# Kernel tuning notes

Measured on AMD Instinct MI355X. Metric: run time of the kernel, lower is better.

The kernel has to match this reference:

```python
import jax, jax.numpy as jnp
import numpy as np

B, N, D_IN, D_HID, D_OUT = 64, 512, 512, 512, 512


def setup_inputs() -> dict:
    key = jax.random.key(0)
    ks = jax.random.split(key, 8)
    gain = 0.02  # xavier_normal_ gain used in reset_parameters_xavier

    def xavier(k, fan_in, fan_out):
        std = gain * np.sqrt(2.0 / (fan_in + fan_out))
        return jax.random.normal(k, (fan_in, fan_out), dtype=jnp.float32) * std

    return {
        "batch_graph": jax.random.normal(ks[0], (B, N, D_IN), dtype=jnp.float32),
        "adj": jax.random.uniform(ks[1], (B, N, N), dtype=jnp.float32),
        "W1": xavier(ks[2], D_IN, D_HID),
        "b1": jnp.zeros((D_HID,), dtype=jnp.float32),
        "W2": xavier(ks[3], D_HID, D_HID),
        "b2": jnp.zeros((D_HID,), dtype=jnp.float32),
        "W3": xavier(ks[4], D_HID, D_OUT),
        "b3": jnp.zeros((D_OUT,), dtype=jnp.float32),
    }


def _normalize_adj(adj):
    # rowsum^-0.5 with inf -> 0 (original: torch.pow then isinf mask)
    rowsum = adj.sum(axis=1)                       # [B, N] (sum over dim 1, as in torch)
    safe = jnp.where(rowsum == 0, 1.0, rowsum)
    r = jnp.where(rowsum == 0, 0.0, safe ** -0.5)  # [B, N]
    # (adj @ D)^T @ D = D @ adj^T @ D with D = diag(r)
    return r[:, :, None] * jnp.swapaxes(adj, 1, 2) * r[:, None, :]


def reference(batch_graph, adj, W1, b1, W2, b2, W3, b3):
    # Block-diagonal big_adj @ big_graph == per-graph batched matmul.
    A = _normalize_adj(adj)  # [B, N, N]

    def gc(x, W, b):
        # support = x @ W ; output = A @ support + b
        return jnp.einsum('bij,bjd->bid', A, x @ W) + b

    # dropout is identity in eval mode (deterministic reference)
    x = jax.nn.relu(gc(batch_graph, W1, b1))
    x = jax.nn.relu(gc(x, W2, b2))
    return gc(x, W3, b3)  # [B, N, D_OUT]
```

## Files before the change

### kernel.cpp

```cpp
#include <hip/hip_runtime.h>
#include <cstdint>
#include <cstddef>

typedef _Float16 f16;
typedef _Float16 f16x4 __attribute__((ext_vector_type(4)));
typedef _Float16 f16x8 __attribute__((ext_vector_type(8)));
typedef float    f32x4 __attribute__((ext_vector_type(4)));

#define NB 64
#define NN 262144

__device__ __forceinline__ void gload_lds16(const void* g, void* l) {
    __builtin_amdgcn_global_load_lds(
        (const __attribute__((address_space(1))) void*)g,
        (__attribute__((address_space(3))) void*)l, 16, 0, 0);
}

__device__ __forceinline__ int SWC(int row, int col) {
    return ((((col >> 2) ^ (row >> 2)) & 15) << 2) | (col & 3);
}

__global__ __launch_bounds__(256)
void k_prep(const float* __restrict__ adj, f16* __restrict__ A_raw,
            float* __restrict__ part,
            const float* __restrict__ W1, const float* __restrict__ W2,
            const float* __restrict__ W3, f16* __restrict__ Wt,
            const float* __restrict__ X0, f16* __restrict__ Xa) {
    __shared__ __align__(16) float t[4096];
    __shared__ float red[4][64];
    const int tid = threadIdx.x;

    for (int u = blockIdx.x; u < 12480; u += 2048) {
        if (u >= 4288) {
            size_t i = ((size_t)(u - 4288) * 256 + tid) * 8;
            float4 v0 = *(const float4*)(X0 + i);
            float4 v1 = *(const float4*)(X0 + i + 4);
            f16x8 o;
            o[0] = (f16)v0.x; o[1] = (f16)v0.y; o[2] = (f16)v0.z; o[3] = (f16)v0.w;
            o[4] = (f16)v1.x; o[5] = (f16)v1.y; o[6] = (f16)v1.z; o[7] = (f16)v1.w;
            *(f16x8*)(Xa + i) = o;
        } else if (u < 4096) {
            const int xcd = u & 7, loc = u >> 3;
            const int b = xcd * 8 + (loc >> 6);
            const int tile = loc & 63;
            const int i0 = (tile >> 3) * 64, j0 = (tile & 7) * 64;
            const int jt = tile & 7;
            const float* ab = adj + (size_t)b * NN;
            #pragma unroll
            for (int s = 0; s < 4; ++s) {
                int rr = s * 16 + (tid >> 4);
                int creal = SWC(rr, (tid & 15) * 4);
                gload_lds16(&ab[(size_t)(j0 + rr) * 512 + i0 + creal],
                            &t[s * 1024 + tid * 4]);
            }
            asm volatile("s_waitcnt vmcnt(0)" ::: "memory");
            __syncthreads();
            {
                int c = tid & 63, g = tid >> 6;
                float sg = 0.f;
                #pragma unroll
                for (int s = 0; s < 16; ++s) {
                    int row = g * 16 + s;
                    sg += t[row * 64 + SWC(row, c)];
                }
                red[g][c] = sg;
            }
            f16* Ab = A_raw + (size_t)b * NN;
            int jq = (tid & 15) * 4;
            int ib = tid >> 4;
            #pragma unroll
            for (int s = 0; s < 4; ++s) {
                int ii = ib + s * 16;
                f16x4 o;
                #pragma unroll
                for (int q = 0; q < 4; ++q)
                    o[q] = (f16)t[(jq + q) * 64 + SWC(jq + q, ii)];
                *(f16x4*)&Ab[(size_t)(i0 + ii) * 512 + j0 + jq] = o;
            }
            __syncthreads();
            if (tid < 64)
                part[((size_t)b * 8 + jt) * 512 + i0 + tid] =
                    red[0][tid] + red[1][tid] + red[2][tid] + red[3][tid];
            __syncthreads();
        } else {
            int cb = u - 4096;
            int z = cb >> 6, rem = cb & 63;
            const float* W = z == 0 ? W1 : (z == 1 ? W2 : W3);
            f16* out = Wt + (size_t)z * NN;
            int k0 = (rem >> 3) * 64, d0 = (rem & 7) * 64;
            int c = tid & 63, r4 = tid >> 6;
            #pragma unroll
            for (int s = 0; s < 16; ++s) {
                int rr = r4 + s * 4;
                t[rr * 64 + SWC(rr, c)] = W[(size_t)(k0 + rr) * 512 + d0 + c];
            }
            __syncthreads();
            int kq = (tid & 15) * 4;
            int db = tid >> 4;
            #pragma unroll
            for (int s = 0; s < 4; ++s) {
                int dd = db + s * 16;
                f16x4 o;
                #pragma unroll
                for (int q = 0; q < 4; ++q)
                    o[q] = (f16)(64.f * t[(kq + q) * 64 + SWC(kq + q, dd)]);
                *(f16x4*)&out[(size_t)(d0 + dd) * 512 + k0 + kq] = o;
            }
            __syncthreads();
        }
    }
}

template<bool BIAS, bool RELU, bool OUTF32, bool RM, bool RN>
__global__ __launch_bounds__(512, 1)
void gemm8(const f16* __restrict__ P, size_t pstr,
           const f16* __restrict__ Qt, size_t qstr,
           void* __restrict__ Cout, size_t cstr,
           const float* __restrict__ bias, const float* __restrict__ part,
           float iscale, float oscale) {
    __shared__ __align__(16) f16 Albuf[2][16384];
    __shared__ __align__(16) f16 Blbuf[2][16384];
    __shared__ float rs_lds[256];

    const int tid  = threadIdx.x;
    const int lane = tid & 63;
    const int wid  = tid >> 6;
    const int wm   = wid >> 2;
    const int wn   = wid & 3;

    const int wg  = blockIdx.x;
    const int swz = (wg & 7) * 32 + (wg >> 3);
    const int b   = swz >> 2;
    const int tt  = swz & 3;
    const int m0  = (tt >> 1) * 256;
    const int n0  = (tt & 1) * 256;

    const f16* Pb = P + (size_t)b * pstr;
    const f16* Qb = Qt + (size_t)b * qstr;

    const int fr = lane & 15, fs = lane >> 4, fx = fr & 7;

    if ((RM || RN) && tid < 256) {
        const float* p = part + (size_t)b * 4096 + (RM ? m0 : n0) + tid;
        float s = 0.f;
        #pragma unroll
        for (int jt = 0; jt < 8; ++jt) s += p[jt * 512];
        rs_lds[tid] = (s > 0.f) ? rsqrtf(s) : 0.f;
    }
    asm volatile("s_waitcnt vmcnt(0)" ::: "memory");

    auto stage_half = [&](const f16* __restrict__ Gb, int row0g, f16* buf, int h, int k0) {
        {
            int row = tid >> 3, sl = tid & 7;
            gload_lds16(Gb + (size_t)(row0g + h * 128 + row) * 512 + k0 + ((sl ^ (row & 7)) * 8),
                        buf + h * 8192 + tid * 8);
        }
        {
            int u = tid + 512;
            int row = u >> 3, sl = u & 7;
            gload_lds16(Gb + (size_t)(row0g + h * 128 + row) * 512 + k0 + ((sl ^ (row & 7)) * 8),
                        buf + h * 8192 + u * 8);
        }
    };

    f32x4 acc[8][4] = {};
    f16x8 af[4][2], bf[2][2];

    stage_half(Qb, n0, &Blbuf[0][0], 0, 0);
    stage_half(Qb, n0, &Blbuf[0][0], 1, 0);
    stage_half(Pb, m0, &Albuf[0][0], 0, 0);
    stage_half(Pb, m0, &Albuf[0][0], 1, 0);

#define LOAD_AF(QM)                                                            \
    _Pragma("unroll") for (int i = 0; i < 4; ++i) {                            \
        int row = wm * 128 + ((QM) * 4 + i) * 16 + fr;                         \
        _Pragma("unroll") for (int k = 0; k < 2; ++k)                          \
            af[i][k] = *(const f16x8*)&Al[row * 64 + ((fs + 4 * k) ^ fx) * 8]; \
    }
#define LOAD_BF(QN)                                                            \
    _Pragma("unroll") for (int j = 0; j < 2; ++j) {                            \
        int row = wn * 64 + ((QN) * 2 + j) * 16 + fr;                          \
        _Pragma("unroll") for (int k = 0; k < 2; ++k)                          \
            bf[j][k] = *(const f16x8*)&Bl[row * 64 + ((fs + 4 * k) ^ fx) * 8]; \
    }
#define PH_SYNC()                                                              \
    __builtin_amdgcn_s_barrier();                                              \
    asm volatile("s_waitcnt lgkmcnt(0)" ::: "memory");                         \
    __builtin_amdgcn_sched_barrier(0);
#define DO_MFMA(QM, QN)                                                        \
    __builtin_amdgcn_s_setprio(1);                                             \
    _Pragma("unroll") for (int i = 0; i < 4; ++i)                              \
        _Pragma("unroll") for (int j = 0; j < 2; ++j)                          \
            _Pragma("unroll") for (int k = 0; k < 2; ++k)                      \
                acc[(QM) * 4 + i][(QN) * 2 + j] =                              \
                    __builtin_amdgcn_mfma_f32_16x16x32_f16(                    \
                        af[i][k], bf[j][k], acc[(QM) * 4 + i][(QN) * 2 + j],   \
                        0, 0, 0);                                              \
    __builtin_amdgcn_s_setprio(0);                                             \
    __builtin_amdgcn_s_barrier();

    for (int t = 0; t < 8; ++t) {
        f16* Al = &Albuf[t & 1][0];
        f16* Bl = &Blbuf[t & 1][0];
        f16* An = &Albuf[(t & 1) ^ 1][0];
        f16* Bn = &Blbuf[(t & 1) ^ 1][0];
        const int kn = (t + 1) * 64;

        asm volatile("s_waitcnt vmcnt(0)" ::: "memory");
        __builtin_amdgcn_s_barrier();

        LOAD_AF(0) LOAD_BF(0)
        if (t < 7) stage_half(Qb, n0, Bn, 0, kn);
        PH_SYNC(); DO_MFMA(0, 0)
        LOAD_BF(1)
        if (t < 7) stage_half(Qb, n0, Bn, 1, kn);
        PH_SYNC(); DO_MFMA(0, 1)
        LOAD_AF(1)
        if (t < 7) stage_half(Pb, m0, An, 0, kn);
        PH_SYNC(); DO_MFMA(1, 1)
        LOAD_BF(0)
        if (t < 7) stage_half(Pb, m0, An, 1, kn);
        PH_SYNC(); DO_MFMA(1, 0)
    }
#undef LOAD_AF
#undef LOAD_BF
#undef PH_SYNC
#undef DO_MFMA

    const int cmb = (lane >> 4) * 4;
    f32x4 rm4[8];
    float rn1[4];
    if (RM) {
        #pragma unroll
        for (int mi = 0; mi < 8; ++mi)
            rm4[mi] = *(const f32x4*)&rs_lds[wm * 128 + mi * 16 + cmb];
    }
    if (RN) {
        #pragma unroll
        for (int ni = 0; ni < 4; ++ni)
            rn1[ni] = rs_lds[wn * 64 + ni * 16 + fr];
    }
    #pragma unroll
    for (int mi = 0; mi < 8; ++mi) {
        #pragma unroll
        for (int ni = 0; ni < 4; ++ni) {
            const int n = n0 + wn * 64 + ni * 16 + fr;
            const int m = m0 + wm * 128 + mi * 16 + cmb;
            float v[4];
            #pragma unroll
            for (int q = 0; q < 4; ++q) {
                float x = acc[mi][ni][q] * iscale;
                if (RM) x *= rm4[mi][q];
                if (RN) x *= rn1[ni];
                if (BIAS) x += bias[m + q];
                if (RELU) x = fmaxf(x, 0.f);
                v[q] = x * oscale;
            }
            if (OUTF32) {
                float* Cb = (float*)Cout + (size_t)b * cstr;
                f32x4 o; o[0] = v[0]; o[1] = v[1]; o[2] = v[2]; o[3] = v[3];
                *(f32x4*)&Cb[(size_t)n * 512 + m] = o;
            } else {
                f16* Cb = (f16*)Cout + (size_t)b * cstr;
                f16x4 o; o[0] = (f16)v[0]; o[1] = (f16)v[1]; o[2] = (f16)v[2]; o[3] = (f16)v[3];
                *(f16x4*)&Cb[(size_t)n * 512 + m] = o;
            }
        }
    }
}

extern "C" void kernel_launch(void* const* d_in, const int* in_sizes, int n_in,
                              void* d_out, int out_size, void* d_ws, size_t ws_size,
                              hipStream_t stream) {
    const float* X0  = (const float*)d_in[0];
    const float* adj = (const float*)d_in[1];
    const float* W1  = (const float*)d_in[2];
    const float* b1  = (const float*)d_in[3];
    const float* W2  = (const float*)d_in[4];
    const float* b2  = (const float*)d_in[5];
    const float* W3  = (const float*)d_in[6];
    const float* b3  = (const float*)d_in[7];

    uint8_t* ws = (uint8_t*)d_ws;
    float* part = (float*)ws;
    f16* Wt1 = (f16*)(ws + (1 << 20));
    f16* A_raw = (f16*)(ws + (1 << 20) + (size_t)3 * NN * 2);
    f16* Xa  = A_raw + (size_t)NB * NN;
    f16* S_t = Xa + (size_t)NB * NN;

    k_prep<<<dim3(2048), dim3(256), 0, stream>>>(adj, A_raw, part, W1, W2, W3, Wt1, X0, Xa);

    dim3 gg(256), gb(512);
    gemm8<false, false, false, true,  false><<<gg, gb, 0, stream>>>(Xa,  (size_t)NN, Wt1, (size_t)0,  S_t, (size_t)NN, nullptr, part, 4.f, 1.f);
    gemm8<true,  true,  false, false, true ><<<gg, gb, 0, stream>>>(S_t, (size_t)NN, A_raw, (size_t)NN, Xa, (size_t)NN, b1, part, 1.f / 256.f, 256.f);
    gemm8<false, false, false, true,  false><<<gg, gb, 0, stream>>>(Xa,  (size_t)NN, Wt1 + NN, (size_t)0,  S_t, (size_t)NN, nullptr, part, 16.f, 1.f);
    gemm8<true,  true,  false, false, true ><<<gg, gb, 0, stream>>>(S_t, (size_t)NN, A_raw, (size_t)NN, Xa, (size_t)NN, b2, part, 1.f / 262144.f, 256.f);
    gemm8<false, false, false, true,  false><<<gg, gb, 0, stream>>>(Xa,  (size_t)NN, Wt1 + 2 * NN, (size_t)0,  S_t, (size_t)NN, nullptr, part, 16.f, 1.f);
    gemm8<true,  false, true,  false, true ><<<gg, gb, 0, stream>>>(S_t, (size_t)NN, A_raw, (size_t)NN, d_out, (size_t)NN, b3, part, 1.f / 262144.f, 1.f);
}
```

Before: 202.1 us.

## Overlap adjacency transpose-conversion with first X@W1 GEMM in one kernel

The adjacency column sums move into the prep kernel as a separate coalesced row-wise reduction into 32 partial chunks. The fp16 transpose of adj now runs in a new kernel, interleaved block-by-block with a smaller 128x128-tile X@W1 GEMM, so the memory-bound transpose and the compute-bound GEMM share the GPU. The aim is to hide the transpose bandwidth behind MFMA work and drop one separate GEMM launch. The cost is more partial sums to reduce in every GEMM epilogue and a smaller GEMM tile that reuses data less.

```diff
diff --git a/kernel.cpp b/kernel.cpp
--- a/kernel.cpp
+++ b/kernel.cpp
@@ -21,69 +21,24 @@
 }
 
 __global__ __launch_bounds__(256)
-void k_prep(const float* __restrict__ adj, f16* __restrict__ A_raw,
-            float* __restrict__ part,
+void k_pre1(const float* __restrict__ adj, float* __restrict__ part,
             const float* __restrict__ W1, const float* __restrict__ W2,
             const float* __restrict__ W3, f16* __restrict__ Wt,
             const float* __restrict__ X0, f16* __restrict__ Xa) {
     __shared__ __align__(16) float t[4096];
-    __shared__ float red[4][64];
     const int tid = threadIdx.x;
 
-    for (int u = blockIdx.x; u < 12480; u += 2048) {
-        if (u >= 4288) {
-            size_t i = ((size_t)(u - 4288) * 256 + tid) * 8;
+    for (int u = blockIdx.x; u < 9408; u += 2048) {
+        if (u < 8192) {
+            size_t i = ((size_t)u * 256 + tid) * 8;
             float4 v0 = *(const float4*)(X0 + i);
             float4 v1 = *(const float4*)(X0 + i + 4);
             f16x8 o;
             o[0] = (f16)v0.x; o[1] = (f16)v0.y; o[2] = (f16)v0.z; o[3] = (f16)v0.w;
             o[4] = (f16)v1.x; o[5] = (f16)v1.y; o[6] = (f16)v1.z; o[7] = (f16)v1.w;
             *(f16x8*)(Xa + i) = o;
-        } else if (u < 4096) {
-            const int xcd = u & 7, loc = u >> 3;
-            const int b = xcd * 8 + (loc >> 6);
-            const int tile = loc & 63;
-            const int i0 = (tile >> 3) * 64, j0 = (tile & 7) * 64;
-            const int jt = tile & 7;
-            const float* ab = adj + (size_t)b * NN;
-            #pragma unroll
-            for (int s = 0; s < 4; ++s) {
-                int rr = s * 16 + (tid >> 4);
-                int creal = SWC(rr, (tid & 15) * 4);
-                gload_lds16(&ab[(size_t)(j0 + rr) * 512 + i0 + creal],
-                            &t[s * 1024 + tid * 4]);
-            }
-            asm volatile("s_waitcnt vmcnt(0)" ::: "memory");
-            __syncthreads();
-            {
-                int c = tid & 63, g = tid >> 6;
-                float sg = 0.f;
-                #pragma unroll
-                for (int s = 0; s < 16; ++s) {
-                    int row = g * 16 + s;
-                    sg += t[row * 64 + SWC(row, c)];
-                }
-                red[g][c] = sg;
-            }
-            f16* Ab = A_raw + (size_t)b * NN;
-            int jq = (tid & 15) * 4;
-            int ib = tid >> 4;
-            #pragma unroll
-            for (int s = 0; s < 4; ++s) {
-                int ii = ib + s * 16;
-                f16x4 o;
-                #pragma unroll
-                for (int q = 0; q < 4; ++q)
-                    o[q] = (f16)t[(jq + q) * 64 + SWC(jq + q, ii)];
-                *(f16x4*)&Ab[(size_t)(i0 + ii) * 512 + j0 + jq] = o;
-            }
-            __syncthreads();
-            if (tid < 64)
-                part[((size_t)b * 8 + jt) * 512 + i0 + tid] =
-                    red[0][tid] + red[1][tid] + red[2][tid] + red[3][tid];
-            __syncthreads();
-        } else {
-            int cb = u - 4096;
+        } else if (u < 8384) {
+            int cb = u - 8192;
             int z = cb >> 6, rem = cb & 63;
             const float* W = z == 0 ? W1 : (z == 1 ? W2 : W3);
             f16* out = Wt + (size_t)z * NN;
@@ -107,6 +62,155 @@
                 *(f16x4*)&out[(size_t)(d0 + dd) * 512 + k0 + kq] = o;
             }
             __syncthreads();
+        } else {
+            int cu = u - 8384;
+            int b = cu >> 4;
+            int rr0 = (cu & 15) * 32 + (tid >> 7) * 16;
+            int c4 = (tid & 127) * 4;
+            const float* ab = adj + (size_t)b * NN + (size_t)rr0 * 512 + c4;
+            f32x4 s = {0.f, 0.f, 0.f, 0.f};
+            #pragma unroll
+            for (int i = 0; i < 16; ++i)
+                s += *(const f32x4*)(ab + (size_t)i * 512);
+            int ch2 = (cu & 15) * 2 + (tid >> 7);
+            *(f32x4*)&part[((size_t)b * 32 + ch2) * 512 + c4] = s;
+        }
+    }
+}
+
+__global__ __launch_bounds__(256, 2)
+void k_g1t(const float* __restrict__ adj, f16* __restrict__ A_raw,
+           const f16* __restrict__ Xa, const f16* __restrict__ Wt1,
+           f16* __restrict__ S_t, const float* __restrict__ part) {
+    __shared__ __align__(16) f16 Plds[2][8192];
+    __shared__ __align__(16) f16 Qlds[2][8192];
+    __shared__ float rs_lds[128];
+    const int bid = blockIdx.x, tid = threadIdx.x;
+    const int q = bid / 5, r5 = bid % 5;
+
+    if (r5 != 0) {
+        const int tix = 4 * q + r5 - 1;
+        const int xcd = tix & 7, loc = tix >> 3;
+        const int b = xcd * 8 + (loc >> 6);
+        const int tile = loc & 63;
+        const int i0 = (tile >> 3) * 64, j0 = (tile & 7) * 64;
+        const float* ab = adj + (size_t)b * NN;
+        float* t = (float*)&Plds[0][0];
+        #pragma unroll
+        for (int s = 0; s < 4; ++s) {
+            int rr = s * 16 + (tid >> 4);
+            int creal = SWC(rr, (tid & 15) * 4);
+            gload_lds16(&ab[(size_t)(j0 + rr) * 512 + i0 + creal],
+                        &t[s * 1024 + tid * 4]);
+        }
+        asm volatile("s_waitcnt vmcnt(0)" ::: "memory");
+        __syncthreads();
+        f16* Ab = A_raw + (size_t)b * NN;
+        int jq = (tid & 15) * 4;
+        int ib = tid >> 4;
+        #pragma unroll
+        for (int s = 0; s < 4; ++s) {
+            int ii = ib + s * 16;
+            f16x4 o;
+            #pragma unroll
+            for (int qq = 0; qq < 4; ++qq)
+                o[qq] = (f16)t[(jq + qq) * 64 + SWC(jq + qq, ii)];
+            *(f16x4*)&Ab[(size_t)(i0 + ii) * 512 + j0 + jq] = o;
+        }
+        return;
+    }
+
+    const int gid  = q;
+    const int lane = tid & 63;
+    const int wid  = tid >> 6;
+    const int wm   = wid >> 1;
+    const int wn   = wid & 1;
+    const int swz = (gid & 7) * 128 + (gid >> 3);
+    const int b   = swz >> 4;
+    const int tt  = swz & 15;
+    const int m0  = (tt >> 2) * 128;
+    const int n0  = (tt & 3) * 128;
+
+    const f16* Pb = Xa + (size_t)b * NN;
+    const f16* Qb = Wt1;
+
+    const int srow = tid >> 3;
+    const int sswz = (tid & 7) ^ (srow & 7);
+    const int fr = lane & 15, fs = lane >> 4, fx = fr & 7;
+
+    auto stage = [&](const f16* __restrict__ Gb, int row0, f16* lds, int k0) {
+        #pragma unroll
+        for (int r = 0; r < 4; ++r) {
+            const f16* src = Gb + (size_t)(row0 + r * 32 + srow) * 512 + k0 + sswz * 8;
+            gload_lds16(src, lds + r * 2048 + tid * 8);
+        }
+    };
+
+    f32x4 acc[4][4] = {};
+    stage(Pb, m0, &Plds[0][0], 0);
+    stage(Qb, n0, &Qlds[0][0], 0);
+
+    if (tid < 128) {
+        const float* p = part + (size_t)b * 16384 + m0 + tid;
+        float s = 0.f;
+        #pragma unroll
+        for (int ch = 0; ch < 32; ++ch) s += p[ch * 512];
+        rs_lds[tid] = (s > 0.f) ? rsqrtf(s) : 0.f;
+    }
+
+    for (int t = 0; t < 8; ++t) {
+        const int nb = t & 1;
+        if (t < 7) {
+            stage(Pb, m0, &Plds[nb ^ 1][0], (t + 1) * 64);
+            stage(Qb, n0, &Qlds[nb ^ 1][0], (t + 1) * 64);
+            asm volatile("s_waitcnt vmcnt(8)" ::: "memory");
+        } else {
+            asm volatile("s_waitcnt vmcnt(0)" ::: "memory");
+        }
+        __builtin_amdgcn_s_barrier();
+
+        const f16* Pl = &Plds[nb][0];
+        const f16* Ql = &Qlds[nb][0];
+        #pragma unroll
+        for (int krep = 0; krep < 2; ++krep) {
+            const int sp = ((fs + krep * 4) ^ fx) * 8;
+            f16x8 af[4], bf[4];
+            #pragma unroll
+            for (int mi = 0; mi < 4; ++mi)
+                af[mi] = *(const f16x8*)&Pl[(wm * 64 + mi * 16 + fr) * 64 + sp];
+            #pragma unroll
+            for (int ni = 0; ni < 4; ++ni)
+                bf[ni] = *(const f16x8*)&Ql[(wn * 64 + ni * 16 + fr) * 64 + sp];
+            __builtin_amdgcn_s_setprio(1);
+            #pragma unroll
+            for (int mi = 0; mi < 4; ++mi)
+                #pragma unroll
+                for (int ni = 0; ni < 4; ++ni)
+                    acc[mi][ni] = __builtin_amdgcn_mfma_f32_16x16x32_f16(
+                        af[mi], bf[ni], acc[mi][ni], 0, 0, 0);
+            __builtin_amdgcn_s_setprio(0);
+        }
+        asm volatile("s_waitcnt lgkmcnt(0)" ::: "memory");
+        __builtin_amdgcn_sched_barrier(0);
+        __builtin_amdgcn_s_barrier();
+    }
+
+    const int cmb = (lane >> 4) * 4;
+    f32x4 rm4[4];
+    #pragma unroll
+    for (int mi = 0; mi < 4; ++mi)
+        rm4[mi] = *(const f32x4*)&rs_lds[wm * 64 + mi * 16 + cmb];
+    #pragma unroll
+    for (int mi = 0; mi < 4; ++mi) {
+        #pragma unroll
+        for (int ni = 0; ni < 4; ++ni) {
+            const int n = n0 + wn * 64 + ni * 16 + fr;
+            const int m = m0 + wm * 64 + mi * 16 + cmb;
+            f16x4 o;
+            #pragma unroll
+            for (int qq = 0; qq < 4; ++qq)
+                o[qq] = (f16)(acc[mi][ni][qq] * 4.f * rm4[mi][qq]);
+            *(f16x4*)&S_t[(size_t)b * NN + (size_t)n * 512 + m] = o;
         }
     }
 }
@@ -141,10 +245,10 @@
     const int fr = lane & 15, fs = lane >> 4, fx = fr & 7;
 
     if ((RM || RN) && tid < 256) {
-        const float* p = part + (size_t)b * 4096 + (RM ? m0 : n0) + tid;
+        const float* p = part + (size_t)b * 16384 + (RM ? m0 : n0) + tid;
         float s = 0.f;
         #pragma unroll
-        for (int jt = 0; jt < 8; ++jt) s += p[jt * 512];
+        for (int ch = 0; ch < 32; ++ch) s += p[ch * 512];
         rs_lds[tid] = (s > 0.f) ? rsqrtf(s) : 0.f;
     }
     asm volatile("s_waitcnt vmcnt(0)" ::: "memory");
@@ -248,13 +352,13 @@
             const int m = m0 + wm * 128 + mi * 16 + cmb;
             float v[4];
             #pragma unroll
-            for (int q = 0; q < 4; ++q) {
-                float x = acc[mi][ni][q] * iscale;
-                if (RM) x *= rm4[mi][q];
+            for (int qq = 0; qq < 4; ++qq) {
+                float x = acc[mi][ni][qq] * iscale;
+                if (RM) x *= rm4[mi][qq];
                 if (RN) x *= rn1[ni];
-                if (BIAS) x += bias[m + q];
+                if (BIAS) x += bias[m + qq];
                 if (RELU) x = fmaxf(x, 0.f);
-                v[q] = x * oscale;
+                v[qq] = x * oscale;
             }
             if (OUTF32) {
                 float* Cb = (float*)Cout + (size_t)b * cstr;
@@ -283,15 +387,15 @@
 
     uint8_t* ws = (uint8_t*)d_ws;
     float* part = (float*)ws;
-    f16* Wt1 = (f16*)(ws + (1 << 20));
-    f16* A_raw = (f16*)(ws + (1 << 20) + (size_t)3 * NN * 2);
+    f16* Wt1 = (f16*)(ws + (4 << 20));
+    f16* A_raw = (f16*)(ws + (4 << 20) + (size_t)3 * NN * 2);
     f16* Xa  = A_raw + (size_t)NB * NN;
     f16* S_t = Xa + (size_t)NB * NN;
 
-    k_prep<<<dim3(2048), dim3(256), 0, stream>>>(adj, A_raw, part, W1, W2, W3, Wt1, X0, Xa);
+    k_pre1<<<dim3(2048), dim3(256), 0, stream>>>(adj, part, W1, W2, W3, Wt1, X0, Xa);
+    k_g1t <<<dim3(5120), dim3(256), 0, stream>>>(adj, A_raw, Xa, Wt1, S_t, part);
 
     dim3 gg(256), gb(512);
-    gemm8<false, false, false, true,  false><<<gg, gb, 0, stream>>>(Xa,  (size_t)NN, Wt1, (size_t)0,  S_t, (size_t)NN, nullptr, part, 4.f, 1.f);
     gemm8<true,  true,  false, false, true ><<<gg, gb, 0, stream>>>(S_t, (size_t)NN, A_raw, (size_t)NN, Xa, (size_t)NN, b1, part, 1.f / 256.f, 256.f);
     gemm8<false, false, false, true,  false><<<gg, gb, 0, stream>>>(Xa,  (size_t)NN, Wt1 + NN, (size_t)0,  S_t, (size_t)NN, nullptr, part, 16.f, 1.f);
     gemm8<true,  true,  false, false, true ><<<gg, gb, 0, stream>>>(S_t, (size_t)NN, A_raw, (size_t)NN, Xa, (size_t)NN, b2, part, 1.f / 262144.f, 256.f);
```

Measured after the change: 217.5 us. +7.6%, slower.
